# Performance work log

Hardware: AMD Instinct MI355X
Metric: run time of the kernel (lower is better)

Reference implementation:

```python
import jax, jax.numpy as jnp
import numpy as np

IN_FEATURES_LS = (8, 16, 32, 64, 128)
OUT_FEATURES = 512
MAX_FEAT = max(IN_FEATURES_LS)


def setup_inputs() -> dict:
    key = jax.random.key(0)
    k_x, k_idx, k_w, k_b = jax.random.split(key, 4)
    B, S = 16, 2048
    x = jax.random.normal(k_x, (B, S, MAX_FEAT), dtype=jnp.float32)
    # actual patch size per token: sample an index into in_features_ls
    idx = jax.random.randint(k_idx, (B, S), 0, len(IN_FEATURES_LS))
    in_feat_size = jnp.array(IN_FEATURES_LS, dtype=jnp.int64)[idx]
    weight = jax.random.normal(k_w, (len(IN_FEATURES_LS), OUT_FEATURES, MAX_FEAT), dtype=jnp.float32) * 0.05
    bias = jax.random.normal(k_b, (len(IN_FEATURES_LS), OUT_FEATURES), dtype=jnp.float32) * 0.05
    return {"x": x, "in_feat_size": in_feat_size, "weight": weight, "bias": bias}


def reference(x, in_feat_size, weight, bias):
    sizes = jnp.asarray(IN_FEATURES_LS)                       # [K]
    # mask padding columns of each expert's weight: [K, max_feat]
    feat_mask = (jnp.arange(MAX_FEAT)[None, :] < sizes[:, None]).astype(x.dtype)
    w = weight * feat_mask[:, None, :]                        # [K, out, max_feat]
    # all K projections computed unconditionally (faithful to original)
    y = jnp.einsum('bsi,koi->bsko', x, w) + bias              # [B, S, K, out]
    sel = (in_feat_size[..., None] == sizes).astype(x.dtype)  # [B, S, K] one-hot
    return jnp.einsum('bsko,bsk->bso', y, sel)                # [B, S, out]
```

## Files before the change

### kernel.cpp

```cpp
#include <hip/hip_runtime.h>

#define NEXP 5
#define MAXF 128
#define NOUT 512
#define PERMOFF 64

typedef __attribute__((ext_vector_type(8))) short short8;
typedef __attribute__((ext_vector_type(4))) float floatx4;

__device__ __forceinline__ ushort f2bf(float f) {
    uint u = __float_as_uint(f);
    u += 0x7FFF + ((u >> 16) & 1);
    return (ushort)(u >> 16);
}


__global__ __launch_bounds__(256) void misl_prep(
    const int* __restrict__ feat, const float* __restrict__ x,
    const float* __restrict__ w, int* __restrict__ ws,
    ushort* __restrict__ wb, ushort* __restrict__ xb, int n, int nb) {
    const int tid = threadIdx.x;
    if ((int)blockIdx.x < nb) {
        __shared__ int lcnt[NEXP], lbase[NEXP];
        if (tid < NEXP) lcnt[tid] = 0;
        __syncthreads();
        const int t = blockIdx.x * 256 + tid;
        int e = 0, r = 0;
        if (t < n) {
            e = __ffs(feat[t]) - 4;
            r = atomicAdd(&lcnt[e], 1);
        }
        __syncthreads();
        if (tid < NEXP) lbase[tid] = atomicAdd(&ws[8 + tid], lcnt[tid]);
        __syncthreads();
        if (t < n) ws[PERMOFF + e * n + lbase[e] + r] = t;
    } else if ((int)blockIdx.x < nb + 160) {
        const int idx = ((int)blockIdx.x - nb) * 256 + tid;
        const int lane = idx & 63, nb16 = (idx >> 6) & 31;
        const int s = (idx >> 11) & 3, e = idx >> 13;
        if (e < NEXP) {
            const int ncol = nb16 * 16 + (lane & 15);
            const int k0 = s * 32 + (lane >> 4) * 8;
            const int K = 8 << e;
            const float* wr = w + ((size_t)e * NOUT + ncol) * MAXF + k0;
            short8 v;
            #pragma unroll
            for (int j = 0; j < 8; ++j)
                v[j] = (short)((k0 + j < K) ? f2bf(wr[j]) : (ushort)0);
            *(short8*)(wb + (size_t)idx * 8) = v;
        }
    } else {
        const int idx = ((int)blockIdx.x - nb - 160) * 256 + tid;
        if (idx < n * 16) {
            const float4 a = *(const float4*)(x + (size_t)idx * 8);
            const float4 c = *(const float4*)(x + (size_t)idx * 8 + 4);
            short8 v;
            v[0] = (short)f2bf(a.x); v[1] = (short)f2bf(a.y);
            v[2] = (short)f2bf(a.z); v[3] = (short)f2bf(a.w);
            v[4] = (short)f2bf(c.x); v[5] = (short)f2bf(c.y);
            v[6] = (short)f2bf(c.z); v[7] = (short)f2bf(c.w);
            *(short8*)(xb + (size_t)idx * 8) = v;
        }
    }
}

template <int NS>
__device__ __forceinline__ void mfma_run(
    const ushort* __restrict__ xb, const ushort* __restrict__ wbe,
    const float* __restrict__ be, const int* __restrict__ tokp, int rem,
    int lane, int n_base, float* __restrict__ out) {
    const int m = lane & 15, q = lane >> 4;
    const int nb16 = n_base >> 4;
    short8 bf[NS][4];
    #pragma unroll
    for (int s = 0; s < NS; ++s)
        #pragma unroll
        for (int bi = 0; bi < 4; ++bi)
            bf[s][bi] = *(const short8*)(wbe + ((size_t)(s * 32 + nb16 + bi) * 64 + lane) * 8);
    float bv[4];
    #pragma unroll
    for (int bi = 0; bi < 4; ++bi) bv[bi] = be[n_base + bi * 16 + m];

    const int trips = (rem + 15) >> 4;
    for (int g = 0; g < trips; ++g) {
        const int base = g * 16;
        const int lim = rem - base;
        const int idx = (m < lim) ? m : lim - 1;
        const int tokv = tokp[base + idx];
        const ushort* xr = xb + (size_t)tokv * MAXF + q * 8;
        floatx4 acc[4];
        #pragma unroll
        for (int bi = 0; bi < 4; ++bi)
            acc[bi] = floatx4{bv[bi], bv[bi], bv[bi], bv[bi]};
        #pragma unroll
        for (int s = 0; s < NS; ++s) {
            const short8 af = *(const short8*)(xr + s * 32);
            #pragma unroll
            for (int bi = 0; bi < 4; ++bi)
                acc[bi] = __builtin_amdgcn_mfma_f32_16x16x32_bf16(af, bf[s][bi], acc[bi], 0, 0, 0);
        }
        #pragma unroll
        for (int r = 0; r < 4; ++r) {
            const int mi = q * 4 + r;
            const int tr = __shfl(tokv, mi, 16);
            if (mi < lim) {
                float* orow = out + (size_t)tr * NOUT + n_base + m;
                #pragma unroll
                for (int bi = 0; bi < 4; ++bi) orow[bi * 16] = acc[bi][r];
            }
        }
    }
}

__global__ __launch_bounds__(512) void misl_main(
    const ushort* __restrict__ xb, const ushort* __restrict__ wb,
    const float* __restrict__ b, const int* __restrict__ ws,
    float* __restrict__ out, int n) {
    const int g = blockIdx.x;
    const int c[NEXP] = {ws[8], ws[9], ws[10], ws[11], ws[12]};

    int gb = 0, e = -1, lgs = 0;
    #pragma unroll
    for (int j = 0; j < NEXP; ++j) {
        const int ee = 4 - j;
        const int ng = (c[ee] + 63) >> 6;
        if (e < 0 && g < gb + ng) { e = ee; lgs = g - gb; }
        gb += ng;
    }
    if (e < 0) return;

    int rem = c[e] - lgs * 64;
    if (rem > 64) rem = 64;
    const int* tokp = ws + PERMOFF + e * n + lgs * 64;
    const int lane = threadIdx.x & 63;
    const int wave = threadIdx.x >> 6;
    const int n_base = wave * 64;
    const ushort* wbe = wb + (size_t)e * 4 * 32 * 64 * 8;
    const float* be = b + e * NOUT;

    switch (e) {
        case 0: mfma_run<1>(xb, wbe, be, tokp, rem, lane, n_base, out); break;
        case 1: mfma_run<1>(xb, wbe, be, tokp, rem, lane, n_base, out); break;
        case 2: mfma_run<1>(xb, wbe, be, tokp, rem, lane, n_base, out); break;
        case 3: mfma_run<2>(xb, wbe, be, tokp, rem, lane, n_base, out); break;
        case 4: mfma_run<4>(xb, wbe, be, tokp, rem, lane, n_base, out); break;
    }
}

extern "C" void kernel_launch(void* const* d_in, const int* in_sizes, int n_in,
                              void* d_out, int out_size, void* d_ws, size_t ws_size,
                              hipStream_t stream) {
    const float* x    = (const float*)d_in[0];
    const int*   feat = (const int*)d_in[1];
    const float* w    = (const float*)d_in[2];
    const float* b    = (const float*)d_in[3];
    float* out = (float*)d_out;
    int*   ws  = (int*)d_ws;

    const int n  = in_sizes[1];
    const int nb = (n + 255) / 256;

    const size_t wb_off = (((size_t)(PERMOFF + (size_t)NEXP * n) * 4) + 255) & ~(size_t)255;
    ushort* wb = (ushort*)((char*)d_ws + wb_off);
    const size_t xb_off = (wb_off + (size_t)NEXP * 4 * 32 * 64 * 8 * 2 + 255) & ~(size_t)255;
    ushort* xb = (ushort*)((char*)d_ws + xb_off);

    hipMemsetAsync(ws, 0, 64 * sizeof(int), stream);
    const int cvb = (n * 16 + 255) / 256;
    misl_prep<<<nb + 160 + cvb, 256, 0, stream>>>(feat, x, w, ws, wb, xb, n, nb);
    misl_main<<<(n + 63) / 64 + NEXP, 512, 0, stream>>>(xb, wb, b, ws, out, n);
}
```

Measured before the change: 98.54 us.

## Fuse routing, conversion and expert GEMM into one per-tile kernel

```diff
diff --git a/kernel.cpp b/kernel.cpp
--- a/kernel.cpp
+++ b/kernel.cpp
@@ -3,7 +3,8 @@
 #define NEXP 5
 #define MAXF 128
 #define NOUT 512
-#define PERMOFF 64
+#define TPB  64
+#define PITCH 136
 
 typedef __attribute__((ext_vector_type(8))) short short8;
 typedef __attribute__((ext_vector_type(4))) float floatx4;
@@ -14,80 +15,38 @@
     return (ushort)(u >> 16);
 }
 
+template <int E>
+__device__ __forceinline__ void run_expert(
+    const ushort* __restrict__ xs, const int* __restrict__ perm,
+    const float* __restrict__ w, const float* __restrict__ b,
+    float* __restrict__ out, int t0, int boff, int c, int lane, int nbase) {
+    constexpr int NS = (E == 4) ? 4 : (E == 3) ? 2 : 1;
+    constexpr int K = 8 << E;
+    const int m = lane & 15, q = lane >> 4;
 
-__global__ __launch_bounds__(256) void misl_prep(
-    const int* __restrict__ feat, const float* __restrict__ x,
-    const float* __restrict__ w, int* __restrict__ ws,
-    ushort* __restrict__ wb, ushort* __restrict__ xb, int n, int nb) {
-    const int tid = threadIdx.x;
-    if ((int)blockIdx.x < nb) {
-        __shared__ int lcnt[NEXP], lbase[NEXP];
-        if (tid < NEXP) lcnt[tid] = 0;
-        __syncthreads();
-        const int t = blockIdx.x * 256 + tid;
-        int e = 0, r = 0;
-        if (t < n) {
-            e = __ffs(feat[t]) - 4;
-            r = atomicAdd(&lcnt[e], 1);
-        }
-        __syncthreads();
-        if (tid < NEXP) lbase[tid] = atomicAdd(&ws[8 + tid], lcnt[tid]);
-        __syncthreads();
-        if (t < n) ws[PERMOFF + e * n + lbase[e] + r] = t;
-    } else if ((int)blockIdx.x < nb + 160) {
-        const int idx = ((int)blockIdx.x - nb) * 256 + tid;
-        const int lane = idx & 63, nb16 = (idx >> 6) & 31;
-        const int s = (idx >> 11) & 3, e = idx >> 13;
-        if (e < NEXP) {
-            const int ncol = nb16 * 16 + (lane & 15);
-            const int k0 = s * 32 + (lane >> 4) * 8;
-            const int K = 8 << e;
-            const float* wr = w + ((size_t)e * NOUT + ncol) * MAXF + k0;
+    short8 bf[NS][4];
+    #pragma unroll
+    for (int s = 0; s < NS; ++s) {
+        const int k0 = s * 32 + q * 8;
+        #pragma unroll
+        for (int bi = 0; bi < 4; ++bi) {
+            const float* wr = w + ((size_t)E * NOUT + (nbase + bi * 16 + m)) * MAXF + k0;
             short8 v;
             #pragma unroll
             for (int j = 0; j < 8; ++j)
                 v[j] = (short)((k0 + j < K) ? f2bf(wr[j]) : (ushort)0);
-            *(short8*)(wb + (size_t)idx * 8) = v;
-        }
-    } else {
-        const int idx = ((int)blockIdx.x - nb - 160) * 256 + tid;
-        if (idx < n * 16) {
-            const float4 a = *(const float4*)(x + (size_t)idx * 8);
-            const float4 c = *(const float4*)(x + (size_t)idx * 8 + 4);
-            short8 v;
-            v[0] = (short)f2bf(a.x); v[1] = (short)f2bf(a.y);
-            v[2] = (short)f2bf(a.z); v[3] = (short)f2bf(a.w);
-            v[4] = (short)f2bf(c.x); v[5] = (short)f2bf(c.y);
-            v[6] = (short)f2bf(c.z); v[7] = (short)f2bf(c.w);
-            *(short8*)(xb + (size_t)idx * 8) = v;
+            bf[s][bi] = v;
         }
     }
-}
-
-template <int NS>
-__device__ __forceinline__ void mfma_run(
-    const ushort* __restrict__ xb, const ushort* __restrict__ wbe,
-    const float* __restrict__ be, const int* __restrict__ tokp, int rem,
-    int lane, int n_base, float* __restrict__ out) {
-    const int m = lane & 15, q = lane >> 4;
-    const int nb16 = n_base >> 4;
-    short8 bf[NS][4];
-    #pragma unroll
-    for (int s = 0; s < NS; ++s)
-        #pragma unroll
-        for (int bi = 0; bi < 4; ++bi)
-            bf[s][bi] = *(const short8*)(wbe + ((size_t)(s * 32 + nb16 + bi) * 64 + lane) * 8);
     float bv[4];
     #pragma unroll
-    for (int bi = 0; bi < 4; ++bi) bv[bi] = be[n_base + bi * 16 + m];
+    for (int bi = 0; bi < 4; ++bi) bv[bi] = b[E * NOUT + nbase + bi * 16 + m];
 
-    const int trips = (rem + 15) >> 4;
-    for (int g = 0; g < trips; ++g) {
-        const int base = g * 16;
-        const int lim = rem - base;
-        const int idx = (m < lim) ? m : lim - 1;
-        const int tokv = tokp[base + idx];
-        const ushort* xr = xb + (size_t)tokv * MAXF + q * 8;
+    for (int o = 0; o < c; o += 16) {
+        const int L = (c - o > 16) ? 16 : (c - o);
+        const int idx = (m < L) ? m : (L - 1);
+        const int row = perm[boff + o + idx];
+        const ushort* xr = xs + row * PITCH + q * 8;
         floatx4 acc[4];
         #pragma unroll
         for (int bi = 0; bi < 4; ++bi)
@@ -102,9 +61,9 @@
         #pragma unroll
         for (int r = 0; r < 4; ++r) {
             const int mi = q * 4 + r;
-            const int tr = __shfl(tokv, mi, 16);
-            if (mi < lim) {
-                float* orow = out + (size_t)tr * NOUT + n_base + m;
+            if (mi < L) {
+                const int trow = perm[boff + o + mi];
+                float* orow = out + ((size_t)(t0 + trow)) * NOUT + nbase + m;
                 #pragma unroll
                 for (int bi = 0; bi < 4; ++bi) orow[bi * 16] = acc[bi][r];
             }
@@ -112,39 +71,72 @@
     }
 }
 
-__global__ __launch_bounds__(512) void misl_main(
-    const ushort* __restrict__ xb, const ushort* __restrict__ wb,
-    const float* __restrict__ b, const int* __restrict__ ws,
+__global__ __launch_bounds__(512) void misl_fused(
+    const float* __restrict__ x, const int* __restrict__ feat,
+    const float* __restrict__ w, const float* __restrict__ b,
     float* __restrict__ out, int n) {
-    const int g = blockIdx.x;
-    const int c[NEXP] = {ws[8], ws[9], ws[10], ws[11], ws[12]};
+    __shared__ ushort xs[TPB * PITCH];
+    __shared__ int perm[TPB];
+    __shared__ int cnt[NEXP];
+    __shared__ int base[NEXP];
 
-    int gb = 0, e = -1, lgs = 0;
-    #pragma unroll
-    for (int j = 0; j < NEXP; ++j) {
-        const int ee = 4 - j;
-        const int ng = (c[ee] + 63) >> 6;
-        if (e < 0 && g < gb + ng) { e = ee; lgs = g - gb; }
-        gb += ng;
+    const int tid = threadIdx.x;
+    const int t0 = blockIdx.x * TPB;
+    const int nt = (n - t0 < TPB) ? (n - t0) : TPB;
+
+    if (tid < NEXP) cnt[tid] = 0;
+
+    const int row = tid >> 3;
+    const int col = (tid & 7) * 16;
+    float4 a0, a1, a2, a3;
+    const bool stage = (row < nt);
+    if (stage) {
+        const float* xp = x + (size_t)t0 * MAXF + tid * 16;
+        a0 = *(const float4*)xp;
+        a1 = *(const float4*)(xp + 4);
+        a2 = *(const float4*)(xp + 8);
+        a3 = *(const float4*)(xp + 12);
     }
-    if (e < 0) return;
+    __syncthreads();
 
-    int rem = c[e] - lgs * 64;
-    if (rem > 64) rem = 64;
-    const int* tokp = ws + PERMOFF + e * n + lgs * 64;
-    const int lane = threadIdx.x & 63;
-    const int wave = threadIdx.x >> 6;
-    const int n_base = wave * 64;
-    const ushort* wbe = wb + (size_t)e * 4 * 32 * 64 * 8;
-    const float* be = b + e * NOUT;
+    int e = 0, r = 0;
+    if (tid < nt) {
+        e = __ffs((uint)feat[t0 + tid]) - 4;
+        r = atomicAdd(&cnt[e], 1);
+    }
+    if (stage) {
+        short8 v0, v1;
+        v0[0] = (short)f2bf(a0.x); v0[1] = (short)f2bf(a0.y);
+        v0[2] = (short)f2bf(a0.z); v0[3] = (short)f2bf(a0.w);
+        v0[4] = (short)f2bf(a1.x); v0[5] = (short)f2bf(a1.y);
+        v0[6] = (short)f2bf(a1.z); v0[7] = (short)f2bf(a1.w);
+        v1[0] = (short)f2bf(a2.x); v1[1] = (short)f2bf(a2.y);
+        v1[2] = (short)f2bf(a2.z); v1[3] = (short)f2bf(a2.w);
+        v1[4] = (short)f2bf(a3.x); v1[5] = (short)f2bf(a3.y);
+        v1[6] = (short)f2bf(a3.z); v1[7] = (short)f2bf(a3.w);
+        *(short8*)(xs + row * PITCH + col)     = v0;
+        *(short8*)(xs + row * PITCH + col + 8) = v1;
+    }
+    __syncthreads();
+    if (tid == 0) {
+        int o = 0;
+        #pragma unroll
+        for (int j = NEXP - 1; j >= 0; --j) { base[j] = o; o += cnt[j]; }
+    }
+    __syncthreads();
+    if (tid < nt) perm[base[e] + r] = tid;
+    __syncthreads();
 
-    switch (e) {
-        case 0: mfma_run<1>(xb, wbe, be, tokp, rem, lane, n_base, out); break;
-        case 1: mfma_run<1>(xb, wbe, be, tokp, rem, lane, n_base, out); break;
-        case 2: mfma_run<1>(xb, wbe, be, tokp, rem, lane, n_base, out); break;
-        case 3: mfma_run<2>(xb, wbe, be, tokp, rem, lane, n_base, out); break;
-        case 4: mfma_run<4>(xb, wbe, be, tokp, rem, lane, n_base, out); break;
-    }
+    const int lane = tid & 63;
+    const int nbase = (tid >> 6) << 6;
+    const int c0 = cnt[0], c1 = cnt[1], c2 = cnt[2], c3 = cnt[3], c4 = cnt[4];
+    const int b0 = base[0], b1 = base[1], b2 = base[2], b3 = base[3], b4 = base[4];
+
+    if (c4) run_expert<4>(xs, perm, w, b, out, t0, b4, c4, lane, nbase);
+    if (c3) run_expert<3>(xs, perm, w, b, out, t0, b3, c3, lane, nbase);
+    if (c2) run_expert<2>(xs, perm, w, b, out, t0, b2, c2, lane, nbase);
+    if (c1) run_expert<1>(xs, perm, w, b, out, t0, b1, c1, lane, nbase);
+    if (c0) run_expert<0>(xs, perm, w, b, out, t0, b0, c0, lane, nbase);
 }
 
 extern "C" void kernel_launch(void* const* d_in, const int* in_sizes, int n_in,
@@ -155,18 +147,8 @@
     const float* w    = (const float*)d_in[2];
     const float* b    = (const float*)d_in[3];
     float* out = (float*)d_out;
-    int*   ws  = (int*)d_ws;
 
-    const int n  = in_sizes[1];
-    const int nb = (n + 255) / 256;
-
-    const size_t wb_off = (((size_t)(PERMOFF + (size_t)NEXP * n) * 4) + 255) & ~(size_t)255;
-    ushort* wb = (ushort*)((char*)d_ws + wb_off);
-    const size_t xb_off = (wb_off + (size_t)NEXP * 4 * 32 * 64 * 8 * 2 + 255) & ~(size_t)255;
-    ushort* xb = (ushort*)((char*)d_ws + xb_off);
-
-    hipMemsetAsync(ws, 0, 64 * sizeof(int), stream);
-    const int cvb = (n * 16 + 255) / 256;
-    misl_prep<<<nb + 160 + cvb, 256, 0, stream>>>(feat, x, w, ws, wb, xb, n, nb);
-    misl_main<<<(n + 63) / 64 + NEXP, 512, 0, stream>>>(xb, wb, b, ws, out, n);
+    const int n = in_sizes[1];
+    const int nblk = (n + TPB - 1) / TPB;
+    misl_fused<<<nblk, 512, 0, stream>>>(x, feat, w, b, out, n);
 }
```

After: 129.4 us. 1.31x slower.

## Fuse x bf16 conversion into main kernel via shared-memory token tile

Applied to the files above, without the earlier changes.

```diff
diff --git a/kernel.cpp b/kernel.cpp
--- a/kernel.cpp
+++ b/kernel.cpp
@@ -4,6 +4,8 @@
 #define MAXF 128
 #define NOUT 512
 #define PERMOFF 64
+#define TPB 64
+#define PITCH 136
 
 typedef __attribute__((ext_vector_type(8))) short short8;
 typedef __attribute__((ext_vector_type(4))) float floatx4;
@@ -16,9 +18,8 @@
 
 
 __global__ __launch_bounds__(256) void misl_prep(
-    const int* __restrict__ feat, const float* __restrict__ x,
-    const float* __restrict__ w, int* __restrict__ ws,
-    ushort* __restrict__ wb, ushort* __restrict__ xb, int n, int nb) {
+    const int* __restrict__ feat, const float* __restrict__ w,
+    int* __restrict__ ws, ushort* __restrict__ wb, int n, int nb) {
     const int tid = threadIdx.x;
     if ((int)blockIdx.x < nb) {
         __shared__ int lcnt[NEXP], lbase[NEXP];
@@ -27,14 +28,14 @@
         const int t = blockIdx.x * 256 + tid;
         int e = 0, r = 0;
         if (t < n) {
-            e = __ffs(feat[t]) - 4;
+            e = __ffs((uint)feat[t]) - 4;
             r = atomicAdd(&lcnt[e], 1);
         }
         __syncthreads();
         if (tid < NEXP) lbase[tid] = atomicAdd(&ws[8 + tid], lcnt[tid]);
         __syncthreads();
         if (t < n) ws[PERMOFF + e * n + lbase[e] + r] = t;
-    } else if ((int)blockIdx.x < nb + 160) {
+    } else {
         const int idx = ((int)blockIdx.x - nb) * 256 + tid;
         const int lane = idx & 63, nb16 = (idx >> 6) & 31;
         const int s = (idx >> 11) & 3, e = idx >> 13;
@@ -49,26 +50,14 @@
                 v[j] = (short)((k0 + j < K) ? f2bf(wr[j]) : (ushort)0);
             *(short8*)(wb + (size_t)idx * 8) = v;
         }
-    } else {
-        const int idx = ((int)blockIdx.x - nb - 160) * 256 + tid;
-        if (idx < n * 16) {
-            const float4 a = *(const float4*)(x + (size_t)idx * 8);
-            const float4 c = *(const float4*)(x + (size_t)idx * 8 + 4);
-            short8 v;
-            v[0] = (short)f2bf(a.x); v[1] = (short)f2bf(a.y);
-            v[2] = (short)f2bf(a.z); v[3] = (short)f2bf(a.w);
-            v[4] = (short)f2bf(c.x); v[5] = (short)f2bf(c.y);
-            v[6] = (short)f2bf(c.z); v[7] = (short)f2bf(c.w);
-            *(short8*)(xb + (size_t)idx * 8) = v;
-        }
     }
 }
 
 template <int NS>
 __device__ __forceinline__ void mfma_run(
-    const ushort* __restrict__ xb, const ushort* __restrict__ wbe,
-    const float* __restrict__ be, const int* __restrict__ tokp, int rem,
-    int lane, int n_base, float* __restrict__ out) {
+    const ushort* __restrict__ xs, const int* __restrict__ tokl,
+    const ushort* __restrict__ wbe, const float* __restrict__ be,
+    int rem, int lane, int n_base, float* __restrict__ out) {
     const int m = lane & 15, q = lane >> 4;
     const int nb16 = n_base >> 4;
     short8 bf[NS][4];
@@ -86,8 +75,7 @@
         const int base = g * 16;
         const int lim = rem - base;
         const int idx = (m < lim) ? m : lim - 1;
-        const int tokv = tokp[base + idx];
-        const ushort* xr = xb + (size_t)tokv * MAXF + q * 8;
+        const ushort* xr = xs + (size_t)(base + idx) * PITCH + q * 8;
         floatx4 acc[4];
         #pragma unroll
         for (int bi = 0; bi < 4; ++bi)
@@ -102,8 +90,8 @@
         #pragma unroll
         for (int r = 0; r < 4; ++r) {
             const int mi = q * 4 + r;
-            const int tr = __shfl(tokv, mi, 16);
             if (mi < lim) {
+                const int tr = tokl[base + mi];
                 float* orow = out + (size_t)tr * NOUT + n_base + m;
                 #pragma unroll
                 for (int bi = 0; bi < 4; ++bi) orow[bi * 16] = acc[bi][r];
@@ -112,10 +100,13 @@
     }
 }
 
-__global__ __launch_bounds__(512) void misl_main(
-    const ushort* __restrict__ xb, const ushort* __restrict__ wb,
+__global__ __launch_bounds__(512, 4) void misl_main(
+    const float* __restrict__ x, const ushort* __restrict__ wb,
     const float* __restrict__ b, const int* __restrict__ ws,
     float* __restrict__ out, int n) {
+    __shared__ ushort xs[TPB * PITCH];
+    __shared__ int tokl[TPB];
+
     const int g = blockIdx.x;
     const int c[NEXP] = {ws[8], ws[9], ws[10], ws[11], ws[12]};
 
@@ -132,18 +123,43 @@
     int rem = c[e] - lgs * 64;
     if (rem > 64) rem = 64;
     const int* tokp = ws + PERMOFF + e * n + lgs * 64;
-    const int lane = threadIdx.x & 63;
-    const int wave = threadIdx.x >> 6;
-    const int n_base = wave * 64;
+
+    const int tid = threadIdx.x;
+    const int row = tid >> 3;
+    const int colu = (tid & 7) * 16;
+    if (row < rem) {
+        const int tok = tokp[row];
+        if ((tid & 7) == 0) tokl[row] = tok;
+        const float* xp = x + (size_t)tok * MAXF + colu;
+        const float4 a0 = *(const float4*)xp;
+        const float4 a1 = *(const float4*)(xp + 4);
+        const float4 a2 = *(const float4*)(xp + 8);
+        const float4 a3 = *(const float4*)(xp + 12);
+        short8 v0, v1;
+        v0[0] = (short)f2bf(a0.x); v0[1] = (short)f2bf(a0.y);
+        v0[2] = (short)f2bf(a0.z); v0[3] = (short)f2bf(a0.w);
+        v0[4] = (short)f2bf(a1.x); v0[5] = (short)f2bf(a1.y);
+        v0[6] = (short)f2bf(a1.z); v0[7] = (short)f2bf(a1.w);
+        v1[0] = (short)f2bf(a2.x); v1[1] = (short)f2bf(a2.y);
+        v1[2] = (short)f2bf(a2.z); v1[3] = (short)f2bf(a2.w);
+        v1[4] = (short)f2bf(a3.x); v1[5] = (short)f2bf(a3.y);
+        v1[6] = (short)f2bf(a3.z); v1[7] = (short)f2bf(a3.w);
+        *(short8*)(xs + (size_t)row * PITCH + colu)     = v0;
+        *(short8*)(xs + (size_t)row * PITCH + colu + 8) = v1;
+    }
+    __syncthreads();
+
+    const int lane = tid & 63;
+    const int n_base = (tid >> 6) * 64;
     const ushort* wbe = wb + (size_t)e * 4 * 32 * 64 * 8;
     const float* be = b + e * NOUT;
 
     switch (e) {
-        case 0: mfma_run<1>(xb, wbe, be, tokp, rem, lane, n_base, out); break;
-        case 1: mfma_run<1>(xb, wbe, be, tokp, rem, lane, n_base, out); break;
-        case 2: mfma_run<1>(xb, wbe, be, tokp, rem, lane, n_base, out); break;
-        case 3: mfma_run<2>(xb, wbe, be, tokp, rem, lane, n_base, out); break;
-        case 4: mfma_run<4>(xb, wbe, be, tokp, rem, lane, n_base, out); break;
+        case 0: mfma_run<1>(xs, tokl, wbe, be, rem, lane, n_base, out); break;
+        case 1: mfma_run<1>(xs, tokl, wbe, be, rem, lane, n_base, out); break;
+        case 2: mfma_run<1>(xs, tokl, wbe, be, rem, lane, n_base, out); break;
+        case 3: mfma_run<2>(xs, tokl, wbe, be, rem, lane, n_base, out); break;
+        case 4: mfma_run<4>(xs, tokl, wbe, be, rem, lane, n_base, out); break;
     }
 }
 
@@ -162,11 +178,8 @@
 
     const size_t wb_off = (((size_t)(PERMOFF + (size_t)NEXP * n) * 4) + 255) & ~(size_t)255;
     ushort* wb = (ushort*)((char*)d_ws + wb_off);
-    const size_t xb_off = (wb_off + (size_t)NEXP * 4 * 32 * 64 * 8 * 2 + 255) & ~(size_t)255;
-    ushort* xb = (ushort*)((char*)d_ws + xb_off);
 
     hipMemsetAsync(ws, 0, 64 * sizeof(int), stream);
-    const int cvb = (n * 16 + 255) / 256;
-    misl_prep<<<nb + 160 + cvb, 256, 0, stream>>>(feat, x, w, ws, wb, xb, n, nb);
-    misl_main<<<(n + 63) / 64 + NEXP, 512, 0, stream>>>(xb, wb, b, ws, out, n);
+    misl_prep<<<nb + 160, 256, 0, stream>>>(feat, w, ws, wb, n, nb);
+    misl_main<<<(n + 63) / 64 + NEXP, 512, 0, stream>>>(x, wb, b, ws, out, n);
 }
```

Result: no change. 98.11 us (-0.4%).
